# Performance work log

Hardware: AMD Instinct MI355X
Metric: run time of the kernel (lower is better)

Reference implementation:

```python
import jax, jax.numpy as jnp
import numpy as np

N_NODES = 100000
N_EDGES = 1600000
N_FEAT = 16
HEADS = 4


def _feast_conv(x, src, dst, U, c, W, b):
    """FeaStConv: q = softmax_h(u^T(x_j - x_i) + c); out_i = mean_j sum_h q_h * (W_h x_j) + b."""
    n = x.shape[0]
    e = src.shape[0]
    xj = x[src]                                   # [E, Fin] gather
    q = jax.nn.softmax(jnp.matmul(xj - x[dst], U) + c, axis=-1)   # [E, H]
    xs = jnp.matmul(xj, W).reshape(e, HEADS, -1)  # [E, H, Fout]
    msg = jnp.einsum('eh,eho->eo', q, xs)         # [E, Fout]
    deg = jax.ops.segment_sum(jnp.ones((e,), x.dtype), dst, num_segments=n)
    agg = jax.ops.segment_sum(msg, dst, num_segments=n)
    return agg / jnp.maximum(deg, 1.0)[:, None] + b


def setup_inputs() -> dict:
    key = jax.random.key(0)
    ks = jax.random.split(key, 32)
    s = 0.1
    d = {
        'x': jax.random.normal(ks[0], (N_NODES, N_FEAT), jnp.float32),
        'edge_index': jax.random.randint(ks[1], (2, N_EDGES), 0, N_NODES, jnp.int32),
        # conv1: 16 -> 16
        'U1': jax.random.normal(ks[2], (N_FEAT, HEADS), jnp.float32) * s,
        'c1': jnp.zeros((HEADS,), jnp.float32),
        'W1': jax.random.normal(ks[3], (N_FEAT, HEADS * 16), jnp.float32) * s,
        'b1': jnp.zeros((16,), jnp.float32),
        # conv2: 16 -> 32
        'U2': jax.random.normal(ks[4], (16, HEADS), jnp.float32) * s,
        'c2': jnp.zeros((HEADS,), jnp.float32),
        'W2': jax.random.normal(ks[5], (16, HEADS * 32), jnp.float32) * s,
        'b2': jnp.zeros((32,), jnp.float32),
        # conv3: 32 -> 64
        'U3': jax.random.normal(ks[6], (32, HEADS), jnp.float32) * s,
        'c3': jnp.zeros((HEADS,), jnp.float32),
        'W3': jax.random.normal(ks[7], (32, HEADS * 64), jnp.float32) * s,
        'b3': jnp.zeros((64,), jnp.float32),
        # linear tail 64->32->16->8->4->1
        'lw1': jax.random.normal(ks[8], (64, 32), jnp.float32) * s,
        'lb1': jnp.zeros((32,), jnp.float32),
        'lw2': jax.random.normal(ks[9], (32, 16), jnp.float32) * s,
        'lb2': jnp.zeros((16,), jnp.float32),
        'lw3': jax.random.normal(ks[10], (16, 8), jnp.float32) * s,
        'lb3': jnp.zeros((8,), jnp.float32),
        'lw4': jax.random.normal(ks[11], (8, 4), jnp.float32) * s,
        'lb4': jnp.zeros((4,), jnp.float32),
        'lw5': jax.random.normal(ks[12], (4, 1), jnp.float32) * s,
        'lb5': jnp.zeros((1,), jnp.float32),
    }
    return d


def reference(x, edge_index, U1, c1, W1, b1, U2, c2, W2, b2, U3, c3, W3, b3,
              lw1, lb1, lw2, lb2, lw3, lb3, lw4, lb4, lw5, lb5):
    src, dst = edge_index[0], edge_index[1]
    h = jax.nn.relu(_feast_conv(x, src, dst, U1, c1, W1, b1))
    h = jax.nn.relu(_feast_conv(h, src, dst, U2, c2, W2, b2))
    h = jax.nn.relu(_feast_conv(h, src, dst, U3, c3, W3, b3))
    # dropout disabled (inference / drop_bool=False): Linear+ReLU tail
    h = jax.nn.relu(jnp.matmul(h, lw1) + lb1)
    h = jax.nn.relu(jnp.matmul(h, lw2) + lb2)
    h = jax.nn.relu(jnp.matmul(h, lw3) + lb3)
    h = jax.nn.relu(jnp.matmul(h, lw4) + lb4)
    return jax.nn.sigmoid(jnp.matmul(h, lw5) + lb5)   # [N, 1]
```

## Files before the change

kernel.cpp:

```cpp
#include <hip/hip_runtime.h>
#include <math.h>

#define N_NODES 100000
#define N_EDGES 1600000
#define HEADS 4
#define NBKT ((N_NODES + 255) / 256)
#define CHUNK_E 4096
#define NCHUNK ((N_EDGES + CHUNK_E - 1) / CHUNK_E)
#define GN ((N_NODES + 255) / 256)

typedef unsigned short ushort_t;
typedef unsigned char  uchar_t;

__device__ __forceinline__ ushort_t f2bf(float x) {
    unsigned u = __float_as_uint(x);
    u += 0x7FFF + ((u >> 16) & 1);
    return (ushort_t)(u >> 16);
}
__device__ __forceinline__ float bf2f(ushort_t v) {
    return __uint_as_float(((unsigned)v) << 16);
}
__device__ __forceinline__ void unpack2(unsigned u, float& lo, float& hi) {
    lo = __uint_as_float(u << 16);
    hi = __uint_as_float(u & 0xffff0000u);
}
__device__ __forceinline__ uchar_t f2fp8(float x) {
    if (x <= 0.0f) return 0;
    unsigned u = __float_as_uint(x) + (1u << 19);
    int e = (int)(u >> 23) - 127 + 15;
    if (e <= 0) return 0;
    if (e > 31) return (uchar_t)255;
    return (uchar_t)((e << 3) | ((u >> 20) & 7));
}
__device__ __forceinline__ float fp8d(uchar_t b) {
    unsigned v = (((unsigned)(b >> 3) + 112u) << 23) | ((unsigned)(b & 7) << 20);
    return (b == 0) ? 0.0f : __uint_as_float(v);
}


__global__ __launch_bounds__(256) void bhist_pcast_kernel(
        const int* __restrict__ dst, int* __restrict__ hist_rows,
        const float* __restrict__ x, const float* __restrict__ U,
        float* __restrict__ p, ushort_t* __restrict__ xbf)
{
    __shared__ int h[NBKT];
    if (blockIdx.x < NCHUNK) {
        for (int i = threadIdx.x; i < NBKT; i += 256) h[i] = 0;
        __syncthreads();
        int base = blockIdx.x * CHUNK_E;
        #pragma unroll
        for (int j = 0; j < CHUNK_E / 256; j++) {
            int e = base + j * 256 + threadIdx.x;
            if (e < N_EDGES) atomicAdd(&h[dst[e] >> 8], 1);
        }
        __syncthreads();
        for (int i = threadIdx.x; i < NBKT; i += 256)
            hist_rows[(size_t)blockIdx.x * NBKT + i] = h[i];
    } else {
        int n = (blockIdx.x - NCHUNK) * 256 + threadIdx.x;
        if (n >= N_NODES) return;
        float a0 = 0, a1 = 0, a2 = 0, a3 = 0;
        const float* hr = x + (size_t)n * 16;
        float xv[16];
        #pragma unroll
        for (int f = 0; f < 16; f++) {
            xv[f] = hr[f];
            a0 += xv[f] * U[f * 4 + 0];
            a1 += xv[f] * U[f * 4 + 1];
            a2 += xv[f] * U[f * 4 + 2];
            a3 += xv[f] * U[f * 4 + 3];
        }
        *(float4*)(p + (size_t)n * 4) = make_float4(a0, a1, a2, a3);
        #pragma unroll
        for (int j = 0; j < 4; j++) {
            ushort4 u;
            u.x = f2bf(xv[4 * j + 0]); u.y = f2bf(xv[4 * j + 1]);
            u.z = f2bf(xv[4 * j + 2]); u.w = f2bf(xv[4 * j + 3]);
            *(ushort4*)(xbf + (size_t)n * 16 + 4 * j) = u;
        }
    }
}


__global__ __launch_bounds__(512) void bscan_kernel(const int* __restrict__ hist_rows,
                                                    int* __restrict__ bucket_base,
                                                    int* __restrict__ bucket_cursor) {
    __shared__ int tmp[512];
    int i = threadIdx.x;
    int v = 0;
    if (i < NBKT)
        for (int r = 0; r < NCHUNK; r++) v += hist_rows[(size_t)r * NBKT + i];
    tmp[i] = v;
    __syncthreads();
    for (int off = 1; off < 512; off <<= 1) {
        int t = (i >= off) ? tmp[i - off] : 0;
        __syncthreads();
        tmp[i] += t;
        __syncthreads();
    }
    int excl = tmp[i] - v;
    if (i < NBKT) { bucket_base[i] = excl; bucket_cursor[i] = excl; }
    if (i == NBKT) bucket_base[NBKT] = N_EDGES;
}


__global__ __launch_bounds__(256) void partition_kernel(const int* __restrict__ src,
                                                        const int* __restrict__ dst,
                                                        int* __restrict__ bucket_cursor,
                                                        int* __restrict__ csr_tmp) {
    constexpr int EPT = CHUNK_E / 256;
    __shared__ int h[NBKT];
    __shared__ int gbase[NBKT];
    __shared__ int rcnt[NBKT];
    for (int i = threadIdx.x; i < NBKT; i += 256) { h[i] = 0; rcnt[i] = 0; }
    __syncthreads();
    int base = blockIdx.x * CHUNK_E;
    int d[EPT], s[EPT];
    #pragma unroll
    for (int j = 0; j < EPT; j++) {
        int e = base + j * 256 + threadIdx.x;
        d[j] = (e < N_EDGES) ? dst[e] : -1;
        s[j] = (e < N_EDGES) ? src[e] : 0;
        if (d[j] >= 0) atomicAdd(&h[d[j] >> 8], 1);
    }
    __syncthreads();
    for (int i = threadIdx.x; i < NBKT; i += 256)
        if (h[i]) gbase[i] = atomicAdd(&bucket_cursor[i], h[i]);
    __syncthreads();
    #pragma unroll
    for (int j = 0; j < EPT; j++) {
        if (d[j] >= 0) {
            int b = d[j] >> 8;
            int r = atomicAdd(&rcnt[b], 1);
            csr_tmp[gbase[b] + r] = ((d[j] & 255) << 20) | s[j];
        }
    }
}


__global__ __launch_bounds__(256) void bucket_build_kernel(const int* __restrict__ bucket_base,
                                                           const int* __restrict__ csr_tmp,
                                                           int* __restrict__ rowptr,
                                                           int* __restrict__ csr_src) {
    __shared__ int cnt[256];
    __shared__ int tscan[256];
    __shared__ int exc[256];
    __shared__ int stage[8192];
    int b = blockIdx.x;
    int rbeg = bucket_base[b], rend = bucket_base[b + 1];
    int sz = rend - rbeg;
    int tid = threadIdx.x;

    cnt[tid] = 0;
    __syncthreads();
    for (int k = rbeg + tid; k < rend; k += 256) atomicAdd(&cnt[csr_tmp[k] >> 20], 1);
    __syncthreads();
    int v = cnt[tid];
    tscan[tid] = v;
    __syncthreads();
    for (int off = 1; off < 256; off <<= 1) {
        int t = (tid >= off) ? tscan[tid - off] : 0;
        __syncthreads();
        tscan[tid] += t;
        __syncthreads();
    }
    int ex = tscan[tid] - v;
    int node = b * 256 + tid;
    if (node < N_NODES) rowptr[node] = rbeg + ex;
    if (b == 0 && tid == 0) rowptr[N_NODES] = N_EDGES;
    exc[tid] = ex;
    cnt[tid] = 0;
    __syncthreads();

    if (sz <= 8192) {
        for (int k = rbeg + tid; k < rend; k += 256) {
            int pk = csr_tmp[k];
            int dl = pk >> 20;
            int r  = atomicAdd(&cnt[dl], 1);
            stage[exc[dl] + r] = pk & ((1 << 20) - 1);
        }
        __syncthreads();
        for (int i = tid; i < sz; i += 256) csr_src[rbeg + i] = stage[i];
    } else {
        for (int k = rbeg + tid; k < rend; k += 256) {
            int pk = csr_tmp[k];
            int dl = pk >> 20;
            int r  = atomicAdd(&cnt[dl], 1);
            csr_src[rbeg + exc[dl] + r] = pk & ((1 << 20) - 1);
        }
    }
}


template<int FIN, int FMT>
__global__ __launch_bounds__(256) void zgather_kernel(
        const int* __restrict__ rowptr, const int* __restrict__ csr_src,
        const float* __restrict__ p, const float* __restrict__ cvec,
        const void* __restrict__ hraw,
        ushort_t* __restrict__ z)
{
    constexpr int LPN   = FIN / 4;
    constexpr int NPB   = 256 / LPN;
    constexpr int CHUNK = 1024;
    __shared__ int    sbeg[NPB + 1];
    __shared__ float4 qs[CHUNK];
    __shared__ int    ssrc[CHUNK];

    const ushort_t* hbf = (const ushort_t*)hraw;
    const uchar_t*  hf8 = (const uchar_t*)hraw;

    int tid  = threadIdx.x;
    int nloc = tid / LPN;
    int fl   = (tid - nloc * LPN) * 4;
    int n0   = blockIdx.x * NPB;
    int n    = n0 + nloc;

    for (int i = tid; i <= NPB; i += 256) {
        int idx = n0 + i;
        sbeg[i] = rowptr[idx > N_NODES ? N_NODES : idx];
    }
    float c0 = cvec[0], c1 = cvec[1], c2 = cvec[2], c3 = cvec[3];
    __syncthreads();

    int BB = sbeg[0], BE = sbeg[NPB];
    int beg = sbeg[nloc], end = sbeg[nloc + 1];

    float4 acc0 = make_float4(0, 0, 0, 0), acc1 = acc0, acc2 = acc0, acc3 = acc0;

    for (int cbase = BB; cbase < BE; cbase += CHUNK) {
        int cend = min(cbase + CHUNK, BE);
        __syncthreads();
        for (int k = cbase + tid; k < cend; k += 256) {
            int s = csr_src[k];
            int lo = 0, hi = NPB;
            while (hi - lo > 1) { int mid = (lo + hi) >> 1; if (k < sbeg[mid]) hi = mid; else lo = mid; }
            float4 ps = *(const float4*)(p + (size_t)s * 4);
            float4 pd = *(const float4*)(p + (size_t)(n0 + lo) * 4);
            float l0 = ps.x - pd.x + c0;
            float l1 = ps.y - pd.y + c1;
            float l2 = ps.z - pd.z + c2;
            float l3 = ps.w - pd.w + c3;
            float m  = fmaxf(fmaxf(l0, l1), fmaxf(l2, l3));
            float e0 = __expf(l0 - m), e1 = __expf(l1 - m);
            float e2 = __expf(l2 - m), e3 = __expf(l3 - m);
            float deg = (float)(sbeg[lo + 1] - sbeg[lo]);
            float inv = 1.0f / (fmaxf(deg, 1.0f) * (e0 + e1 + e2 + e3));
            qs[k - cbase]   = make_float4(e0 * inv, e1 * inv, e2 * inv, e3 * inv);
            ssrc[k - cbase] = s;
        }
        __syncthreads();
        int kb = (beg > cbase ? beg : cbase) - cbase;
        int ke = (end < cend ? end : cend) - cbase;
        int k = kb;
        for (; k + 4 <= ke; k += 4) {
            float xv[4][4];
            if (FMT == 0) {
                uint2 r[4];
                #pragma unroll
                for (int j = 0; j < 4; j++)
                    r[j] = *(const uint2*)(hbf + (size_t)ssrc[k + j] * FIN + fl);
                #pragma unroll
                for (int j = 0; j < 4; j++) {
                    unpack2(r[j].x, xv[j][0], xv[j][1]);
                    unpack2(r[j].y, xv[j][2], xv[j][3]);
                }
            } else {
                unsigned r[4];
                #pragma unroll
                for (int j = 0; j < 4; j++)
                    r[j] = *(const unsigned*)(hf8 + (size_t)ssrc[k + j] * FIN + fl);
                #pragma unroll
                for (int j = 0; j < 4; j++) {
                    xv[j][0] = fp8d((uchar_t)(r[j] & 255));
                    xv[j][1] = fp8d((uchar_t)((r[j] >> 8) & 255));
                    xv[j][2] = fp8d((uchar_t)((r[j] >> 16) & 255));
                    xv[j][3] = fp8d((uchar_t)(r[j] >> 24));
                }
            }
            #pragma unroll
            for (int j = 0; j < 4; j++) {
                float4 q = qs[k + j];
                acc0.x += q.x * xv[j][0]; acc0.y += q.x * xv[j][1];
                acc0.z += q.x * xv[j][2]; acc0.w += q.x * xv[j][3];
                acc1.x += q.y * xv[j][0]; acc1.y += q.y * xv[j][1];
                acc1.z += q.y * xv[j][2]; acc1.w += q.y * xv[j][3];
                acc2.x += q.z * xv[j][0]; acc2.y += q.z * xv[j][1];
                acc2.z += q.z * xv[j][2]; acc2.w += q.z * xv[j][3];
                acc3.x += q.w * xv[j][0]; acc3.y += q.w * xv[j][1];
                acc3.z += q.w * xv[j][2]; acc3.w += q.w * xv[j][3];
            }
        }
        for (; k < ke; k++) {
            float x0, x1, x2, x3;
            if (FMT == 0) {
                uint2 r = *(const uint2*)(hbf + (size_t)ssrc[k] * FIN + fl);
                unpack2(r.x, x0, x1);
                unpack2(r.y, x2, x3);
            } else {
                unsigned r = *(const unsigned*)(hf8 + (size_t)ssrc[k] * FIN + fl);
                x0 = fp8d((uchar_t)(r & 255));
                x1 = fp8d((uchar_t)((r >> 8) & 255));
                x2 = fp8d((uchar_t)((r >> 16) & 255));
                x3 = fp8d((uchar_t)(r >> 24));
            }
            float4 q = qs[k];
            acc0.x += q.x * x0; acc0.y += q.x * x1; acc0.z += q.x * x2; acc0.w += q.x * x3;
            acc1.x += q.y * x0; acc1.y += q.y * x1; acc1.z += q.y * x2; acc1.w += q.y * x3;
            acc2.x += q.z * x0; acc2.y += q.z * x1; acc2.z += q.z * x2; acc2.w += q.z * x3;
            acc3.x += q.w * x0; acc3.y += q.w * x1; acc3.z += q.w * x2; acc3.w += q.w * x3;
        }
    }

    if (n < N_NODES) {
        size_t base = (size_t)n * (4 * FIN) + fl;
        ushort4 u;
        u.x = f2bf(acc0.x); u.y = f2bf(acc0.y); u.z = f2bf(acc0.z); u.w = f2bf(acc0.w);
        *(ushort4*)(z + base) = u;
        u.x = f2bf(acc1.x); u.y = f2bf(acc1.y); u.z = f2bf(acc1.z); u.w = f2bf(acc1.w);
        *(ushort4*)(z + base + FIN) = u;
        u.x = f2bf(acc2.x); u.y = f2bf(acc2.y); u.z = f2bf(acc2.z); u.w = f2bf(acc2.w);
        *(ushort4*)(z + base + 2 * FIN) = u;
        u.x = f2bf(acc3.x); u.y = f2bf(acc3.y); u.z = f2bf(acc3.z); u.w = f2bf(acc3.w);
        *(ushort4*)(z + base + 3 * FIN) = u;
    }
}


template<int FIN, int FOUT, int MODE>
__global__ __launch_bounds__(256, 4) void post_kernel(
        const ushort_t* __restrict__ z,
        const float* __restrict__ W,
        const float* __restrict__ b,
        ushort_t* __restrict__ out_bf,
        uchar_t* __restrict__ out_f8,
        const float* __restrict__ Unext,
        float* __restrict__ pnext)
{
    constexpr int K   = 4 * FIN;
    constexpr int OL  = FOUT / 4;
    constexpr int NPB = 4 * (256 / OL);
    constexpr int WSZ = FIN * 4 * FOUT;
    constexpr bool PNEXT = (MODE != 0);
    __shared__ float Wp[WSZ];
    __shared__ float htile[PNEXT ? NPB * FOUT : 1];
    __shared__ float Uloc[PNEXT ? FOUT * 4 : 1];
    for (int i = threadIdx.x; i < WSZ; i += 256) {
        int f = i / (4 * FOUT);
        int r = i - f * (4 * FOUT);
        int h = r / FOUT;
        int o = r - h * FOUT;
        Wp[(h * FIN + f) * FOUT + o] = W[i];
    }
    if (PNEXT) {
        for (int i = threadIdx.x; i < FOUT * 4; i += 256) Uloc[i] = Unext[i];
    }
    __syncthreads();

    int ol = threadIdx.x % OL;
    int g  = threadIdx.x / OL;
    int n0 = blockIdx.x * NPB + g * 4;

    float4 bv = *(const float4*)(b + 4 * ol);
    float4 acc[4];
    const ushort_t* zr[4];
    #pragma unroll
    for (int j = 0; j < 4; j++) {
        acc[j] = make_float4(0.f, 0.f, 0.f, 0.f);
        int nn = n0 + j; if (nn > N_NODES - 1) nn = N_NODES - 1;
        zr[j] = z + (size_t)nn * K;
    }

    #pragma unroll 2
    for (int kq = 0; kq < K / 4; kq++) {
        float zv[4][4];
        #pragma unroll
        for (int j = 0; j < 4; j++) {
            ushort4 zu = *(const ushort4*)(zr[j] + 4 * kq);
            zv[j][0] = bf2f(zu.x); zv[j][1] = bf2f(zu.y);
            zv[j][2] = bf2f(zu.z); zv[j][3] = bf2f(zu.w);
        }
        #pragma unroll
        for (int jj = 0; jj < 4; jj++) {
            float4 wv = *(const float4*)(Wp + (4 * kq + jj) * FOUT + 4 * ol);
            #pragma unroll
            for (int j = 0; j < 4; j++) {
                float s = zv[j][jj];
                acc[j].x += s * wv.x;
                acc[j].y += s * wv.y;
                acc[j].z += s * wv.z;
                acc[j].w += s * wv.w;
            }
        }
    }

    #pragma unroll
    for (int j = 0; j < 4; j++) {
        int nn = n0 + j;
        float4 r;
        r.x = fmaxf(acc[j].x + bv.x, 0.0f);
        r.y = fmaxf(acc[j].y + bv.y, 0.0f);
        r.z = fmaxf(acc[j].z + bv.z, 0.0f);
        r.w = fmaxf(acc[j].w + bv.w, 0.0f);
        if (PNEXT)
            *(float4*)(htile + (g * 4 + j) * FOUT + 4 * ol) = r;
        if (nn < N_NODES) {
            if (MODE == 2) {
                uchar_t u0 = f2fp8(r.x), u1 = f2fp8(r.y), u2 = f2fp8(r.z), u3 = f2fp8(r.w);
                unsigned pk = (unsigned)u0 | ((unsigned)u1 << 8) |
                              ((unsigned)u2 << 16) | ((unsigned)u3 << 24);
                *(unsigned*)(out_f8 + (size_t)nn * FOUT + 4 * ol) = pk;
            } else {
                ushort4 u;
                u.x = f2bf(r.x); u.y = f2bf(r.y); u.z = f2bf(r.z); u.w = f2bf(r.w);
                *(ushort4*)(out_bf + (size_t)nn * FOUT + 4 * ol) = u;
            }
        }
    }

    if (PNEXT) {
        __syncthreads();
        int tid = threadIdx.x;
        if (tid < NPB) {
            int nn = blockIdx.x * NPB + tid;
            if (nn < N_NODES) {
                float a0 = 0, a1 = 0, a2 = 0, a3 = 0;
                const float* hr = htile + tid * FOUT;
                #pragma unroll
                for (int f = 0; f < FOUT; f++) {
                    float xv = hr[f];
                    a0 += xv * Uloc[f * 4 + 0];
                    a1 += xv * Uloc[f * 4 + 1];
                    a2 += xv * Uloc[f * 4 + 2];
                    a3 += xv * Uloc[f * 4 + 3];
                }
                *(float4*)(pnext + (size_t)nn * 4) = make_float4(a0, a1, a2, a3);
            }
        }
    }
}


__global__ __launch_bounds__(256) void tail_kernel(
        const ushort_t* __restrict__ h,
        const float* __restrict__ lw1, const float* __restrict__ lb1,
        const float* __restrict__ lw2, const float* __restrict__ lb2,
        const float* __restrict__ lw3, const float* __restrict__ lb3,
        const float* __restrict__ lw4, const float* __restrict__ lb4,
        const float* __restrict__ lw5, const float* __restrict__ lb5,
        float* __restrict__ out)
{
    __shared__ float w1[64 * 32], w2[32 * 16], w3[16 * 8], w4[8 * 4], w5[4];
    __shared__ float B1[32], B2[16], B3[8], B4[4], B5[1];
    for (int i = threadIdx.x; i < 64 * 32; i += blockDim.x) w1[i] = lw1[i];
    for (int i = threadIdx.x; i < 32 * 16; i += blockDim.x) w2[i] = lw2[i];
    for (int i = threadIdx.x; i < 16 * 8;  i += blockDim.x) w3[i] = lw3[i];
    for (int i = threadIdx.x; i < 8 * 4;   i += blockDim.x) w4[i] = lw4[i];
    for (int i = threadIdx.x; i < 4;       i += blockDim.x) w5[i] = lw5[i];
    for (int i = threadIdx.x; i < 32; i += blockDim.x) B1[i] = lb1[i];
    for (int i = threadIdx.x; i < 16; i += blockDim.x) B2[i] = lb2[i];
    for (int i = threadIdx.x; i < 8;  i += blockDim.x) B3[i] = lb3[i];
    for (int i = threadIdx.x; i < 4;  i += blockDim.x) B4[i] = lb4[i];
    if (threadIdx.x == 0) B5[0] = lb5[0];
    __syncthreads();

    int n = blockIdx.x * blockDim.x + threadIdx.x;
    if (n >= N_NODES) return;

    float a[64];
    const uint4* hrow = (const uint4*)(h + (size_t)n * 64);
    #pragma unroll
    for (int j = 0; j < 8; j++) {
        uint4 v = hrow[j];
        unpack2(v.x, a[8 * j + 0], a[8 * j + 1]);
        unpack2(v.y, a[8 * j + 2], a[8 * j + 3]);
        unpack2(v.z, a[8 * j + 4], a[8 * j + 5]);
        unpack2(v.w, a[8 * j + 6], a[8 * j + 7]);
    }

    float t1[32];
    for (int o = 0; o < 32; o++) {
        float acc = B1[o];
        #pragma unroll
        for (int i = 0; i < 64; i++) acc += a[i] * w1[i * 32 + o];
        t1[o] = fmaxf(acc, 0.0f);
    }
    float t2[16];
    for (int o = 0; o < 16; o++) {
        float acc = B2[o];
        #pragma unroll
        for (int i = 0; i < 32; i++) acc += t1[i] * w2[i * 16 + o];
        t2[o] = fmaxf(acc, 0.0f);
    }
    float t3[8];
    for (int o = 0; o < 8; o++) {
        float acc = B3[o];
        #pragma unroll
        for (int i = 0; i < 16; i++) acc += t2[i] * w3[i * 8 + o];
        t3[o] = fmaxf(acc, 0.0f);
    }
    float t4[4];
    for (int o = 0; o < 4; o++) {
        float acc = B4[o];
        #pragma unroll
        for (int i = 0; i < 8; i++) acc += t3[i] * w4[i * 4 + o];
        t4[o] = fmaxf(acc, 0.0f);
    }
    float zf = B5[0];
    #pragma unroll
    for (int i = 0; i < 4; i++) zf += t4[i] * w5[i];
    out[n] = 1.0f / (1.0f + expf(-zf));
}


extern "C" void kernel_launch(void* const* d_in, const int* in_sizes, int n_in,
                              void* d_out, int out_size, void* d_ws, size_t ws_size,
                              hipStream_t stream) {
    const float* x   = (const float*)d_in[0];
    const int*   ei  = (const int*)d_in[1];
    const int*   src = ei;
    const int*   dst = ei + N_EDGES;
    const float* U1 = (const float*)d_in[2];  const float* c1 = (const float*)d_in[3];
    const float* W1 = (const float*)d_in[4];  const float* b1 = (const float*)d_in[5];
    const float* U2 = (const float*)d_in[6];  const float* c2 = (const float*)d_in[7];
    const float* W2 = (const float*)d_in[8];  const float* b2 = (const float*)d_in[9];
    const float* U3 = (const float*)d_in[10]; const float* c3 = (const float*)d_in[11];
    const float* W3 = (const float*)d_in[12]; const float* b3 = (const float*)d_in[13];
    const float* lw1 = (const float*)d_in[14]; const float* lb1 = (const float*)d_in[15];
    const float* lw2 = (const float*)d_in[16]; const float* lb2 = (const float*)d_in[17];
    const float* lw3 = (const float*)d_in[18]; const float* lb3 = (const float*)d_in[19];
    const float* lw4 = (const float*)d_in[20]; const float* lb4 = (const float*)d_in[21];
    const float* lw5 = (const float*)d_in[22]; const float* lb5 = (const float*)d_in[23];

    char* ws = (char*)d_ws;
    size_t off = 0;
    auto alloc = [&](size_t bytes) -> void* {
        void* ptr = (void*)(ws + off);
        off += (bytes + 255) & ~(size_t)255;
        return ptr;
    };
    int*      hist_rows     = (int*)alloc((size_t)NCHUNK * NBKT * 4);
    int*      bucket_base   = (int*)alloc((size_t)(NBKT + 1) * 4);
    int*      bucket_cursor = (int*)alloc((size_t)NBKT * 4);
    int*      csr_tmp       = (int*)alloc((size_t)N_EDGES * 4);
    int*      rowptr        = (int*)alloc(((size_t)N_NODES + 1) * 4);
    int*      csr_src       = (int*)alloc((size_t)N_EDGES * 4);
    float*    p             = (float*)alloc((size_t)N_NODES * 4 * 4);
    ushort_t* z             = (ushort_t*)alloc((size_t)N_NODES * 128 * 2);
    ushort_t* xbf           = (ushort_t*)alloc((size_t)N_NODES * 16 * 2);
    ushort_t* h1bf          = (ushort_t*)alloc((size_t)N_NODES * 16 * 2);
    uchar_t*  h2f8          = (uchar_t*)alloc((size_t)N_NODES * 32);
    ushort_t* h3bf          = (ushort_t*)alloc((size_t)N_NODES * 64 * 2);
    (void)ws_size;

    const int B = 256;

    bhist_pcast_kernel<<<NCHUNK + GN, B, 0, stream>>>(dst, hist_rows, x, U1, p, xbf);
    bscan_kernel<<<1, 512, 0, stream>>>(hist_rows, bucket_base, bucket_cursor);
    partition_kernel<<<NCHUNK, B, 0, stream>>>(src, dst, bucket_cursor, csr_tmp);
    bucket_build_kernel<<<NBKT, B, 0, stream>>>(bucket_base, csr_tmp, rowptr, csr_src);

    const int ZG16 = (N_NODES + 63) / 64;
    const int ZG32 = (N_NODES + 31) / 32;
    const int NPB1 = 4 * (256 / (16 / 4));
    const int NPB2 = 4 * (256 / (32 / 4));
    const int NPB3 = 4 * (256 / (64 / 4));

    zgather_kernel<16, 0><<<ZG16, B, 0, stream>>>(rowptr, csr_src, p, c1, xbf, z);
    post_kernel<16, 16, 1><<<(N_NODES + NPB1 - 1) / NPB1, B, 0, stream>>>(
        z, W1, b1, h1bf, nullptr, U2, p);

    zgather_kernel<16, 0><<<ZG16, B, 0, stream>>>(rowptr, csr_src, p, c2, h1bf, z);
    post_kernel<16, 32, 2><<<(N_NODES + NPB2 - 1) / NPB2, B, 0, stream>>>(
        z, W2, b2, nullptr, h2f8, U3, p);

    zgather_kernel<32, 1><<<ZG32, B, 0, stream>>>(rowptr, csr_src, p, c3, h2f8, z);
    post_kernel<32, 64, 0><<<(N_NODES + NPB3 - 1) / NPB3, B, 0, stream>>>(
        z, W3, b3, h3bf, nullptr, nullptr, nullptr);

    tail_kernel<<<GN, B, 0, stream>>>(h3bf, lw1, lb1, lw2, lb2, lw3, lb3,
                                      lw4, lb4, lw5, lb5, (float*)d_out);
}
```

Measured before the change: 337.5 us.

## Parallelize bucket histogram reduction and pack dst-local index into CSR entries

The single-block bucket scan used to sum all 391 chunk histogram rows serially. That sum now runs in a new multi-block kernel that reduces groups of rows with atomics, and the scan only reads the totals. The CSR source entries also keep the packed destination-local bits, so the z-gather kernel takes each edge's node directly instead of binary-searching rowptr, and it reads destination p values from shared memory. This adds one kernel launch and an extra block that zeroes the counters.

```diff
diff --git a/kernel.cpp b/kernel.cpp
--- a/kernel.cpp
+++ b/kernel.cpp
@@ -8,6 +8,8 @@
 #define CHUNK_E 4096
 #define NCHUNK ((N_EDGES + CHUNK_E - 1) / CHUNK_E)
 #define GN ((N_NODES + 255) / 256)
+#define SUM_ROWS 16
+#define NRB ((NCHUNK + SUM_ROWS - 1) / SUM_ROWS)
 
 typedef unsigned short ushort_t;
 typedef unsigned char  uchar_t;
@@ -41,7 +43,8 @@
 __global__ __launch_bounds__(256) void bhist_pcast_kernel(
         const int* __restrict__ dst, int* __restrict__ hist_rows,
         const float* __restrict__ x, const float* __restrict__ U,
-        float* __restrict__ p, ushort_t* __restrict__ xbf)
+        float* __restrict__ p, ushort_t* __restrict__ xbf,
+        int* __restrict__ bucket_cnt)
 {
     __shared__ int h[NBKT];
     if (blockIdx.x < NCHUNK) {
@@ -56,7 +59,7 @@
         __syncthreads();
         for (int i = threadIdx.x; i < NBKT; i += 256)
             hist_rows[(size_t)blockIdx.x * NBKT + i] = h[i];
-    } else {
+    } else if (blockIdx.x < NCHUNK + GN) {
         int n = (blockIdx.x - NCHUNK) * 256 + threadIdx.x;
         if (n >= N_NODES) return;
         float a0 = 0, a1 = 0, a2 = 0, a3 = 0;
@@ -78,18 +81,30 @@
             u.z = f2bf(xv[4 * j + 2]); u.w = f2bf(xv[4 * j + 3]);
             *(ushort4*)(xbf + (size_t)n * 16 + 4 * j) = u;
         }
-    }
-}
-
-
-__global__ __launch_bounds__(512) void bscan_kernel(const int* __restrict__ hist_rows,
+    } else {
+        for (int i = threadIdx.x; i < NBKT; i += 256) bucket_cnt[i] = 0;
+    }
+}
+
+
+__global__ __launch_bounds__(256) void ksum_kernel(const int* __restrict__ hist_rows,
+                                                   int* __restrict__ bucket_cnt) {
+    int r0 = blockIdx.x * SUM_ROWS;
+    int r1 = min(r0 + SUM_ROWS, NCHUNK);
+    for (int i = threadIdx.x; i < NBKT; i += 256) {
+        int v = 0;
+        for (int r = r0; r < r1; r++) v += hist_rows[(size_t)r * NBKT + i];
+        if (v) atomicAdd(&bucket_cnt[i], v);
+    }
+}
+
+
+__global__ __launch_bounds__(512) void bscan_kernel(const int* __restrict__ bucket_cnt,
                                                     int* __restrict__ bucket_base,
                                                     int* __restrict__ bucket_cursor) {
     __shared__ int tmp[512];
     int i = threadIdx.x;
-    int v = 0;
-    if (i < NBKT)
-        for (int r = 0; r < NCHUNK; r++) v += hist_rows[(size_t)r * NBKT + i];
+    int v = (i < NBKT) ? bucket_cnt[i] : 0;
     tmp[i] = v;
     __syncthreads();
     for (int off = 1; off < 512; off <<= 1) {
@@ -177,7 +192,7 @@
             int pk = csr_tmp[k];
             int dl = pk >> 20;
             int r  = atomicAdd(&cnt[dl], 1);
-            stage[exc[dl] + r] = pk & ((1 << 20) - 1);
+            stage[exc[dl] + r] = pk;
         }
         __syncthreads();
         for (int i = tid; i < sz; i += 256) csr_src[rbeg + i] = stage[i];
@@ -186,7 +201,7 @@
             int pk = csr_tmp[k];
             int dl = pk >> 20;
             int r  = atomicAdd(&cnt[dl], 1);
-            csr_src[rbeg + exc[dl] + r] = pk & ((1 << 20) - 1);
+            csr_src[rbeg + exc[dl] + r] = pk;
         }
     }
 }
@@ -203,6 +218,7 @@
     constexpr int NPB   = 256 / LPN;
     constexpr int CHUNK = 1024;
     __shared__ int    sbeg[NPB + 1];
+    __shared__ float4 pds[NPB];
     __shared__ float4 qs[CHUNK];
     __shared__ int    ssrc[CHUNK];
 
@@ -214,11 +230,16 @@
     int fl   = (tid - nloc * LPN) * 4;
     int n0   = blockIdx.x * NPB;
     int n    = n0 + nloc;
+    int dbase = n0 & 255;
 
     for (int i = tid; i <= NPB; i += 256) {
         int idx = n0 + i;
         sbeg[i] = rowptr[idx > N_NODES ? N_NODES : idx];
     }
+    for (int i = tid; i < NPB; i += 256) {
+        int idx = n0 + i;
+        pds[i] = *(const float4*)(p + (size_t)(idx < N_NODES ? idx : N_NODES - 1) * 4);
+    }
     float c0 = cvec[0], c1 = cvec[1], c2 = cvec[2], c3 = cvec[3];
     __syncthreads();
 
@@ -231,11 +252,11 @@
         int cend = min(cbase + CHUNK, BE);
         __syncthreads();
         for (int k = cbase + tid; k < cend; k += 256) {
-            int s = csr_src[k];
-            int lo = 0, hi = NPB;
-            while (hi - lo > 1) { int mid = (lo + hi) >> 1; if (k < sbeg[mid]) hi = mid; else lo = mid; }
+            int pk = csr_src[k];
+            int s  = pk & ((1 << 20) - 1);
+            int nl = (pk >> 20) - dbase;
             float4 ps = *(const float4*)(p + (size_t)s * 4);
-            float4 pd = *(const float4*)(p + (size_t)(n0 + lo) * 4);
+            float4 pd = pds[nl];
             float l0 = ps.x - pd.x + c0;
             float l1 = ps.y - pd.y + c1;
             float l2 = ps.z - pd.z + c2;
@@ -243,7 +264,7 @@
             float m  = fmaxf(fmaxf(l0, l1), fmaxf(l2, l3));
             float e0 = __expf(l0 - m), e1 = __expf(l1 - m);
             float e2 = __expf(l2 - m), e3 = __expf(l3 - m);
-            float deg = (float)(sbeg[lo + 1] - sbeg[lo]);
+            float deg = (float)(sbeg[nl + 1] - sbeg[nl]);
             float inv = 1.0f / (fmaxf(deg, 1.0f) * (e0 + e1 + e2 + e3));
             qs[k - cbase]   = make_float4(e0 * inv, e1 * inv, e2 * inv, e3 * inv);
             ssrc[k - cbase] = s;
@@ -539,6 +560,7 @@
         return ptr;
     };
     int*      hist_rows     = (int*)alloc((size_t)NCHUNK * NBKT * 4);
+    int*      bucket_cnt    = (int*)alloc((size_t)(NBKT + 1) * 4);
     int*      bucket_base   = (int*)alloc((size_t)(NBKT + 1) * 4);
     int*      bucket_cursor = (int*)alloc((size_t)NBKT * 4);
     int*      csr_tmp       = (int*)alloc((size_t)N_EDGES * 4);
@@ -554,8 +576,10 @@
 
     const int B = 256;
 
-    bhist_pcast_kernel<<<NCHUNK + GN, B, 0, stream>>>(dst, hist_rows, x, U1, p, xbf);
-    bscan_kernel<<<1, 512, 0, stream>>>(hist_rows, bucket_base, bucket_cursor);
+    bhist_pcast_kernel<<<NCHUNK + GN + 1, B, 0, stream>>>(dst, hist_rows, x, U1, p, xbf,
+                                                          bucket_cnt);
+    ksum_kernel<<<NRB, B, 0, stream>>>(hist_rows, bucket_cnt);
+    bscan_kernel<<<1, 512, 0, stream>>>(bucket_cnt, bucket_base, bucket_cursor);
     partition_kernel<<<NCHUNK, B, 0, stream>>>(src, dst, bucket_cursor, csr_tmp);
     bucket_build_kernel<<<NBKT, B, 0, stream>>>(bucket_base, csr_tmp, rowptr, csr_src);
 
```

Result: faster. 326.3 us (-3.3%).
